# Kernel tuning notes

Measured on AMD Instinct MI355X. Metric: run time of the kernel, lower is better.

Reference implementation:

```python
import jax, jax.numpy as jnp
import numpy as np

N = 100000   # nodes
E = 1600000  # edges
F = 128      # input/hidden dim
C = 3        # classes
G = 64       # graphs in batch


def setup_inputs() -> dict:
    key = jax.random.key(0)
    ks = jax.random.split(key, 12)
    s = 1.0 / np.sqrt(F)
    return {
        "x": jax.random.normal(ks[0], (N, F), dtype=jnp.float32),
        "edge_index": jax.random.randint(ks[1], (2, E), 0, N, dtype=jnp.int64),
        "batch": jnp.sort(jax.random.randint(ks[2], (N,), 0, G, dtype=jnp.int64)),
        "W1": jax.random.normal(ks[3], (F, F), dtype=jnp.float32) * s,
        "b1": jnp.zeros((F,), dtype=jnp.float32),
        "W2": jax.random.normal(ks[4], (F, F), dtype=jnp.float32) * s,
        "b2": jnp.zeros((F,), dtype=jnp.float32),
        "W3": jax.random.normal(ks[5], (F, F), dtype=jnp.float32) * s,
        "b3": jnp.zeros((F,), dtype=jnp.float32),
        "Wc": jax.random.normal(ks[6], (F, C), dtype=jnp.float32) * s,
        "bc": jnp.zeros((C,), dtype=jnp.float32),
    }


def reference(x, edge_index, batch, W1, b1, W2, b2, W3, b3, Wc, bc):
    n = x.shape[0]
    src, dst = edge_index[0], edge_index[1]
    # GCN adds self-loops: A_hat = A + I
    loops = jnp.arange(n, dtype=src.dtype)
    src_a = jnp.concatenate([src, loops])
    dst_a = jnp.concatenate([dst, loops])
    # symmetric normalization D^-1/2 (A+I) D^-1/2 (in-degree incl. self-loop)
    deg = jax.ops.segment_sum(jnp.ones_like(dst_a, dtype=x.dtype), dst_a, num_segments=n)
    dis = jnp.where(deg > 0, jax.lax.rsqrt(deg), 0.0)
    norm = dis[src_a] * dis[dst_a]  # [E+N]

    def gcn_conv(h, W, b):
        h = h @ W                                    # [N, F']
        msg = h[src_a] * norm[:, None]               # gather + scale
        agg = jax.ops.segment_sum(msg, dst_a, num_segments=n)  # scatter-add
        return agg + b

    h = jax.nn.relu(gcn_conv(x, W1, b1))   # dropout = identity in eval mode
    h = jax.nn.relu(gcn_conv(h, W2, b2))
    h = jax.nn.relu(gcn_conv(h, W3, b3))

    # global_mean_pool over graph ids
    sums = jax.ops.segment_sum(h, batch, num_segments=G)
    cnt = jax.ops.segment_sum(jnp.ones((n,), dtype=h.dtype), batch, num_segments=G)
    pooled = sums / jnp.maximum(cnt, 1.0)[:, None]
    return pooled @ Wc + bc
```

## Files before the change

kernel.cpp:

```cpp
#include <hip/hip_runtime.h>
#include <cstdint>
#include <cstddef>

#define FDIM 128
#define CHUNK 4096
#define BSHIFT 8
#define BMASK 255
#define MAXB 512

typedef unsigned short ushort_t;
typedef __attribute__((ext_vector_type(8))) short short8;
typedef __attribute__((ext_vector_type(4))) float floatx4;

__device__ inline ushort_t f2bf(float f) {
  unsigned u = __float_as_uint(f);
  u += 0x7fffu + ((u >> 16) & 1u);
  return (ushort_t)(u >> 16);
}
__device__ inline float bf2f(ushort_t h) {
  return __uint_as_float((unsigned)h << 16);
}

__global__ __launch_bounds__(256) void k_histw(const int* __restrict__ dst, int e,
                                               int nb, int* __restrict__ chunkHist,
                                               int nch,
                                               const float* __restrict__ W1,
                                               const float* __restrict__ W2,
                                               const float* __restrict__ W3,
                                               ushort_t* __restrict__ wsw,
                                               int* __restrict__ counter) {
  if (blockIdx.x >= (unsigned)nch) {
    int b = blockIdx.x - nch;
    if (b == 0 && threadIdx.x == 0) *counter = 0;
    const float* W = (b == 0) ? W1 : (b == 1) ? W2 : W3;
    ushort_t* o = wsw + (size_t)b * 16384;
    for (int idx = threadIdx.x; idx < 16384; idx += 256) {
      int j = idx & 7;
      int lane = (idx >> 3) & 63;
      int ct = (idx >> 9) & 7;
      int kc = idx >> 12;
      int k = kc * 32 + (lane >> 4) * 8 + j;
      int col = (lane & 15) * 8 + ct;
      o[idx] = f2bf(W[k * FDIM + col]);
    }
    return;
  }
  __shared__ int h[MAXB];
  int c = blockIdx.x;
  int base = c * CHUNK;
  int end = min(base + CHUNK, e);
  for (int i = threadIdx.x; i < nb; i += 256) h[i] = 0;
  __syncthreads();
  for (int i = base + threadIdx.x; i < end; i += 256)
    atomicAdd(&h[dst[i] >> BSHIFT], 1);
  __syncthreads();
  for (int b = threadIdx.x; b < nb; b += 256)
    chunkHist[(size_t)c * nb + b] = h[b];
}

__global__ __launch_bounds__(512) void k_scan1(const int* __restrict__ chunkHist,
                                               int nchunks, int nb,
                                               int* __restrict__ chunkOff,
                                               int* __restrict__ bucketTotal,
                                               int* __restrict__ bucketBase,
                                               int* __restrict__ counter) {
  __shared__ int sb[512];
  int b = blockIdx.x;
  int t = threadIdx.x;
  int base = 0;
  for (int c0 = 0; c0 < nchunks; c0 += 512) {
    int c = c0 + t;
    int v = (c < nchunks) ? chunkHist[(size_t)c * nb + b] : 0;
    int x = v;
    sb[t] = x;
    __syncthreads();
    for (int off = 1; off < 512; off <<= 1) {
      int y = (t >= off) ? sb[t - off] : 0;
      __syncthreads();
      x += y;
      sb[t] = x;
      __syncthreads();
    }
    if (c < nchunks) chunkOff[(size_t)c * nb + b] = base + x - v;
    int tileTot = sb[511];
    __syncthreads();
    base += tileTot;
  }
  if (t == 0) {
    bucketTotal[b] = base;
    bucketBase[b] = atomicAdd(counter, base);
  }
}

__global__ __launch_bounds__(256) void k_bin(const int* __restrict__ src,
                                             const int* __restrict__ dst, int e, int nb,
                                             const int* __restrict__ chunkHist,
                                             const int* __restrict__ chunkOff,
                                             const int* __restrict__ bucketBase,
                                             unsigned* __restrict__ binned) {
  __shared__ unsigned sortedL[CHUNK];
  __shared__ int gtarget[CHUNK];
  __shared__ int lbase[MAXB], lcur[MAXB], gbase[MAXB];
  __shared__ int stmp[256];
  int c = blockIdx.x;
  int base = c * CHUNK;
  int end = min(base + CHUNK, e);
  for (int i = threadIdx.x; i < nb; i += 256) {
    lbase[i] = chunkHist[(size_t)c * nb + i];
    gbase[i] = bucketBase[i] + chunkOff[(size_t)c * nb + i];
  }
  __syncthreads();
  int carry = 0;
  for (int i0 = 0; i0 < nb; i0 += 256) {
    int i = i0 + threadIdx.x;
    int v = (i < nb) ? lbase[i] : 0;
    int x = v;
    stmp[threadIdx.x] = x;
    __syncthreads();
    for (int off = 1; off < 256; off <<= 1) {
      int y = (threadIdx.x >= off) ? stmp[threadIdx.x - off] : 0;
      __syncthreads();
      x += y;
      stmp[threadIdx.x] = x;
      __syncthreads();
    }
    if (i < nb) lbase[i] = carry + x - v;
    int tileTot = stmp[255];
    __syncthreads();
    carry += tileTot;
  }
  for (int i = threadIdx.x; i < nb; i += 256) lcur[i] = lbase[i];
  __syncthreads();
  for (int i = base + threadIdx.x; i < end; i += 256) {
    int d = dst[i];
    int sv = src[i];
    int b = d >> BSHIFT;
    int slot = atomicAdd(&lcur[b], 1);
    sortedL[slot] = ((unsigned)sv << BSHIFT) | (unsigned)(d & BMASK);
    gtarget[slot] = gbase[b] + (slot - lbase[b]);
  }
  __syncthreads();
  for (int i = threadIdx.x; i < end - base; i += 256)
    binned[gtarget[i]] = sortedL[i];
}

__global__ __launch_bounds__(256) void k_fill2(const unsigned* __restrict__ binned,
                                               const int* __restrict__ bucketBase,
                                               const int* __restrict__ bucketTotal,
                                               int n,
                                               int* __restrict__ rowStart,
                                               int* __restrict__ deg,
                                               float* __restrict__ dis,
                                               unsigned* __restrict__ colPacked) {
  __shared__ int h[256], sb[256], cur[256];
  int b = blockIdx.x;
  int s0 = bucketBase[b], s1 = s0 + bucketTotal[b];
  int nodeBase = b << BSHIFT;
  int t = threadIdx.x;
  h[t] = 0;
  __syncthreads();
  for (int i = s0 + t; i < s1; i += 256) atomicAdd(&h[binned[i] & BMASK], 1);
  __syncthreads();
  int v = h[t];
  int x = v;
  sb[t] = x;
  __syncthreads();
  for (int off = 1; off < 256; off <<= 1) {
    int y = (t >= off) ? sb[t - off] : 0;
    __syncthreads();
    x += y;
    sb[t] = x;
    __syncthreads();
  }
  int start = s0 + x - v;
  cur[t] = start;
  int node = nodeBase + t;
  if (node < n) {
    rowStart[node] = start;
    deg[node] = v;
    dis[node] = rsqrtf((float)(v + 1));
  }
  __syncthreads();
  for (int i = s0 + t; i < s1; i += 256) {
    unsigned en = binned[i];
    int slot = atomicAdd(&cur[en & BMASK], 1);
    colPacked[slot] = en >> BSHIFT;
  }
}

template <int INBF, int EDGW>
__global__ __launch_bounds__(256) void k_mm(const void* __restrict__ Ain,
                                            const ushort_t* __restrict__ Wsw,
                                            ushort_t* __restrict__ O, int n, int mmb,
                                            unsigned* __restrict__ colPacked, int e,
                                            const float* __restrict__ dis) {
  if (EDGW && blockIdx.x >= (unsigned)mmb) {
    int base = (blockIdx.x - mmb) * 2048 + threadIdx.x;
    for (int k = 0; k < 8; ++k) {
      int i = base + k * 256;
      if (i < e) {
        unsigned p = colPacked[i];
        colPacked[i] = p | ((unsigned)f2bf(dis[p]) << 17);
      }
    }
    return;
  }
  __shared__ ushort_t Bs[16384];
  int tid = threadIdx.x;
  for (int q = tid; q < 2048; q += 256)
    ((uint4*)Bs)[q] = ((const uint4*)Wsw)[q];
  __syncthreads();

  int w = tid >> 6;
  int lane = tid & 63;
  int quad = lane >> 4;
  int l15 = lane & 15;
  int rb = blockIdx.x * 128 + w * 32;
  const float* Af = (const float*)Ain;
  const ushort_t* Ab = (const ushort_t*)Ain;

  int row0 = rb + l15;
  int row1 = rb + 16 + l15;
  bool v0 = row0 < n, v1 = row1 < n;

  floatx4 acc[2][8];
#pragma unroll
  for (int rt = 0; rt < 2; ++rt)
#pragma unroll
    for (int ct = 0; ct < 8; ++ct) acc[rt][ct] = floatx4{0.f, 0.f, 0.f, 0.f};

#pragma unroll
  for (int kc = 0; kc < 4; ++kc) {
    int k0 = kc * 32 + quad * 8;
    short8 a0 = short8{0, 0, 0, 0, 0, 0, 0, 0};
    short8 a1 = short8{0, 0, 0, 0, 0, 0, 0, 0};
    if (INBF) {
      if (v0) a0 = *(const short8*)&Ab[(size_t)row0 * FDIM + k0];
      if (v1) a1 = *(const short8*)&Ab[(size_t)row1 * FDIM + k0];
    } else {
      if (v0) {
        float4 f0 = *(const float4*)&Af[(size_t)row0 * FDIM + k0];
        float4 f1 = *(const float4*)&Af[(size_t)row0 * FDIM + k0 + 4];
        a0 = short8{(short)f2bf(f0.x), (short)f2bf(f0.y), (short)f2bf(f0.z),
                    (short)f2bf(f0.w), (short)f2bf(f1.x), (short)f2bf(f1.y),
                    (short)f2bf(f1.z), (short)f2bf(f1.w)};
      }
      if (v1) {
        float4 f0 = *(const float4*)&Af[(size_t)row1 * FDIM + k0];
        float4 f1 = *(const float4*)&Af[(size_t)row1 * FDIM + k0 + 4];
        a1 = short8{(short)f2bf(f0.x), (short)f2bf(f0.y), (short)f2bf(f0.z),
                    (short)f2bf(f0.w), (short)f2bf(f1.x), (short)f2bf(f1.y),
                    (short)f2bf(f1.z), (short)f2bf(f1.w)};
      }
    }
#pragma unroll
    for (int ct = 0; ct < 8; ++ct) {
      short8 bf = *(const short8*)&Bs[((kc * 8 + ct) * 64 + lane) * 8];
      acc[0][ct] = __builtin_amdgcn_mfma_f32_16x16x32_bf16(a0, bf, acc[0][ct], 0, 0, 0);
      acc[1][ct] = __builtin_amdgcn_mfma_f32_16x16x32_bf16(a1, bf, acc[1][ct], 0, 0, 0);
    }
  }

#pragma unroll
  for (int rt = 0; rt < 2; ++rt) {
#pragma unroll
    for (int i = 0; i < 4; ++i) {
      int row = rb + rt * 16 + quad * 4 + i;
      if (row < n) {
        uint4 pk;
        pk.x = (unsigned)f2bf(acc[rt][0][i]) | ((unsigned)f2bf(acc[rt][1][i]) << 16);
        pk.y = (unsigned)f2bf(acc[rt][2][i]) | ((unsigned)f2bf(acc[rt][3][i]) << 16);
        pk.z = (unsigned)f2bf(acc[rt][4][i]) | ((unsigned)f2bf(acc[rt][5][i]) << 16);
        pk.w = (unsigned)f2bf(acc[rt][6][i]) | ((unsigned)f2bf(acc[rt][7][i]) << 16);
        *(uint4*)&O[(size_t)row * FDIM + l15 * 8] = pk;
      }
    }
  }
}

__global__ __launch_bounds__(256) void k_agg(const ushort_t* __restrict__ Hin,
                                             ushort_t* __restrict__ Hout,
                                             const int* __restrict__ rowStart,
                                             const int* __restrict__ degE,
                                             const unsigned* __restrict__ colPacked,
                                             const float* __restrict__ dis,
                                             const float* __restrict__ bias, int n) {
  int node = blockIdx.x * 8 + (threadIdx.x >> 5);
  int lane = threadIdx.x & 31;
  if (node >= n) return;
  const uint2* hin = (const uint2*)Hin;
  float di = dis[node];
  uint2 su = hin[(size_t)node * 32 + lane];
  float ws = di * di;
  float a0 = ws * __uint_as_float(su.x << 16);
  float a1 = ws * __uint_as_float(su.x & 0xffff0000u);
  float a2 = ws * __uint_as_float(su.y << 16);
  float a3 = ws * __uint_as_float(su.y & 0xffff0000u);
  int s0 = rowStart[node], cnt = degE[node];
  const unsigned* __restrict__ cp = colPacked + s0;

  int j = 0;
  int main8 = cnt & ~7;
  if (main8) {
    unsigned pv[8];
#pragma unroll
    for (int k = 0; k < 8; ++k) pv[k] = cp[k];
    for (;;) {
      uint2 u[8];
#pragma unroll
      for (int k = 0; k < 8; ++k)
        u[k] = hin[(size_t)(pv[k] & 0x1ffffu) * 32 + lane];
      int jn = j + 8;
      bool more = jn < main8;
      unsigned pn[8];
      if (more) {
#pragma unroll
        for (int k = 0; k < 8; ++k) pn[k] = cp[jn + k];
      }
#pragma unroll
      for (int k = 0; k < 8; ++k) {
        float w = di * __uint_as_float((pv[k] >> 17) << 16);
        a0 += w * __uint_as_float(u[k].x << 16);
        a1 += w * __uint_as_float(u[k].x & 0xffff0000u);
        a2 += w * __uint_as_float(u[k].y << 16);
        a3 += w * __uint_as_float(u[k].y & 0xffff0000u);
      }
      j = jn;
      if (!more) break;
#pragma unroll
      for (int k = 0; k < 8; ++k) pv[k] = pn[k];
    }
  }
  if (j + 4 <= cnt) {
    unsigned pv[4];
#pragma unroll
    for (int k = 0; k < 4; ++k) pv[k] = cp[j + k];
    uint2 u[4];
#pragma unroll
    for (int k = 0; k < 4; ++k)
      u[k] = hin[(size_t)(pv[k] & 0x1ffffu) * 32 + lane];
#pragma unroll
    for (int k = 0; k < 4; ++k) {
      float w = di * __uint_as_float((pv[k] >> 17) << 16);
      a0 += w * __uint_as_float(u[k].x << 16);
      a1 += w * __uint_as_float(u[k].x & 0xffff0000u);
      a2 += w * __uint_as_float(u[k].y << 16);
      a3 += w * __uint_as_float(u[k].y & 0xffff0000u);
    }
    j += 4;
  }
  for (; j < cnt; ++j) {
    unsigned pv = cp[j];
    int sidx = (int)(pv & 0x1ffffu);
    float w = di * __uint_as_float((pv >> 17) << 16);
    uint2 u = hin[(size_t)sidx * 32 + lane];
    a0 += w * __uint_as_float(u.x << 16);
    a1 += w * __uint_as_float(u.x & 0xffff0000u);
    a2 += w * __uint_as_float(u.y << 16);
    a3 += w * __uint_as_float(u.y & 0xffff0000u);
  }
  float4 b = ((const float4*)bias)[lane];
  a0 = fmaxf(a0 + b.x, 0.f);
  a1 = fmaxf(a1 + b.y, 0.f);
  a2 = fmaxf(a2 + b.z, 0.f);
  a3 = fmaxf(a3 + b.w, 0.f);
  uint2 o;
  o.x = (unsigned)f2bf(a0) | ((unsigned)f2bf(a1) << 16);
  o.y = (unsigned)f2bf(a2) | ((unsigned)f2bf(a3) << 16);
  ((uint2*)Hout)[(size_t)node * 32 + lane] = o;
}


__device__ inline int lower_bound_batch(const int* __restrict__ batch, int n, int g) {
  int lo = 0, hi = n;
  while (lo < hi) {
    int mid = (lo + hi) >> 1;
    if (batch[mid] < g) lo = mid + 1;
    else hi = mid;
  }
  return lo;
}

__global__ __launch_bounds__(128) void k_pool(const ushort_t* __restrict__ H,
                                              const int* __restrict__ batch, int n,
                                              float* __restrict__ partials,
                                              int g_count) {
  __shared__ int se[2];
  int g = blockIdx.x >> 4;
  int c = blockIdx.x & 15;
  if (threadIdx.x < 2)
    se[threadIdx.x] = lower_bound_batch(batch, n, g + (int)threadIdx.x);
  __syncthreads();
  int s = se[0], e = se[1];
  int chunk = (e - s + 15) >> 4;
  int ns = s + c * chunk;
  int ne = min(ns + chunk, e);
  float acc = 0.f;
  for (int i = ns; i < ne; ++i) acc += bf2f(H[(size_t)i * FDIM + threadIdx.x]);
  partials[((size_t)g * 16 + c) * FDIM + threadIdx.x] = acc;
}

__global__ __launch_bounds__(128) void k_final(const float* __restrict__ partials,
                                               const int* __restrict__ batch, int n,
                                               const float* __restrict__ Wc,
                                               const float* __restrict__ bc,
                                               float* __restrict__ out, int g_count) {
  __shared__ int se[2];
  __shared__ float red[6];
  int t = threadIdx.x;
  int g = blockIdx.x;
  if (t < 2) se[t] = lower_bound_batch(batch, n, g + t);
  __syncthreads();
  float inv = 1.0f / (float)max(se[1] - se[0], 1);
  float s = 0.f;
#pragma unroll
  for (int p = 0; p < 16; ++p) s += partials[((size_t)g * 16 + p) * FDIM + t];
  s *= inv;
#pragma unroll
  for (int c = 0; c < 3; ++c) {
    float v = s * Wc[t * 3 + c];
#pragma unroll
    for (int off = 1; off < 64; off <<= 1) v += __shfl_xor(v, off);
    if ((t & 63) == 0) red[(t >> 6) * 3 + c] = v;
  }
  __syncthreads();
  if (t < 3) out[g * 3 + t] = red[t] + red[3 + t] + bc[t];
}


extern "C" void kernel_launch(void* const* d_in, const int* in_sizes, int n_in,
                              void* d_out, int out_size, void* d_ws, size_t ws_size,
                              hipStream_t stream) {
  const float* x = (const float*)d_in[0];
  const int* edge = (const int*)d_in[1];
  const int* batch = (const int*)d_in[2];
  const float* W1 = (const float*)d_in[3];
  const float* b1 = (const float*)d_in[4];
  const float* W2 = (const float*)d_in[5];
  const float* b2 = (const float*)d_in[6];
  const float* W3 = (const float*)d_in[7];
  const float* b3 = (const float*)d_in[8];
  const float* Wc = (const float*)d_in[9];
  const float* bc = (const float*)d_in[10];
  float* out = (float*)d_out;

  const int N = in_sizes[0] / FDIM;
  const int E = in_sizes[1] / 2;
  const int G = out_size / 3;
  const int* src = edge;
  const int* dst = edge + E;

  const int NCH = (E + CHUNK - 1) / CHUNK;
  const int NB = (N + (1 << BSHIFT) - 1) >> BSHIFT;

  char* ws = (char*)d_ws;
  size_t off = 0;
  auto carve = [&](size_t bytes) -> void* {
    void* p = ws + off;
    off = (off + bytes + 255) & ~(size_t)255;
    return p;
  };
  ushort_t* h0 = (ushort_t*)carve((size_t)N * FDIM * 2);
  ushort_t* h1 = (ushort_t*)carve((size_t)N * FDIM * 2);
  unsigned* colPacked = (unsigned*)carve((size_t)E * 4);
  unsigned* binned = (unsigned*)carve((size_t)E * 4);
  int* chunkHist = (int*)carve((size_t)NCH * NB * 4);
  int* chunkOff = (int*)carve((size_t)NCH * NB * 4);
  int* bucketTotal = (int*)carve((size_t)NB * 4);
  int* bucketBase = (int*)carve((size_t)NB * 4);
  int* counter = (int*)carve(256);
  int* rowStart = (int*)carve((size_t)N * 4);
  int* deg = (int*)carve((size_t)N * 4);
  float* dis = (float*)carve((size_t)N * 4);
  float* partials = (float*)carve((size_t)G * 16 * FDIM * 4);
  ushort_t* wsw = (ushort_t*)carve((size_t)3 * 16384 * 2);
  (void)n_in;
  (void)ws_size;

  k_histw<<<NCH + 3, 256, 0, stream>>>(dst, E, NB, chunkHist, NCH, W1, W2, W3, wsw,
                                       counter);
  k_scan1<<<NB, 512, 0, stream>>>(chunkHist, NCH, NB, chunkOff, bucketTotal,
                                  bucketBase, counter);
  k_bin<<<NCH, 256, 0, stream>>>(src, dst, E, NB, chunkHist, chunkOff, bucketBase,
                                 binned);
  k_fill2<<<NB, 256, 0, stream>>>(binned, bucketBase, bucketTotal, N, rowStart, deg,
                                  dis, colPacked);

  int mmb = (N + 127) / 128;
  int ewb = (E + 2047) / 2048;
  int aggb = (N + 7) / 8;
  k_mm<0, 1><<<mmb + ewb, 256, 0, stream>>>(x, wsw, h0, N, mmb, colPacked, E, dis);
  k_agg<<<aggb, 256, 0, stream>>>(h0, h1, rowStart, deg, colPacked, dis, b1, N);
  k_mm<1, 0><<<mmb, 256, 0, stream>>>(h1, wsw + 16384, h0, N, mmb, nullptr, 0,
                                      nullptr);
  k_agg<<<aggb, 256, 0, stream>>>(h0, h1, rowStart, deg, colPacked, dis, b2, N);
  k_mm<1, 0><<<mmb, 256, 0, stream>>>(h1, wsw + 32768, h0, N, mmb, nullptr, 0,
                                      nullptr);
  k_agg<<<aggb, 256, 0, stream>>>(h0, h1, rowStart, deg, colPacked, dis, b3, N);

  k_pool<<<G * 16, 128, 0, stream>>>(h1, batch, N, partials, G);
  k_final<<<G, 128, 0, stream>>>(partials, batch, N, Wc, bc, out, G);
}
```

Baseline: 417.3 us.

## Fuse GCN aggregation with next layer's matmul via LDS-staged tile

Adds k_fagg, which aggregates neighbor features for 128 nodes per block into a swizzled LDS tile, then multiplies that tile by the next layer's weights with MFMA. It replaces the separate agg and mm kernels for layers 1 and 2. This removes a global write and read of the intermediate node features plus two launches per layer. In exchange each block needs 64KB of LDS and 512 threads, which limits occupancy during the latency-bound gather phase.

After: 435.6 us. 1.04x slower.

```diff
diff --git a/kernel.cpp b/kernel.cpp
--- a/kernel.cpp
+++ b/kernel.cpp
@@ -274,6 +274,144 @@
         pk.w = (unsigned)f2bf(acc[rt][6][i]) | ((unsigned)f2bf(acc[rt][7][i]) << 16);
         *(uint4*)&O[(size_t)row * FDIM + l15 * 8] = pk;
       }
+    }
+  }
+}
+
+__global__ __launch_bounds__(512, 4) void k_fagg(
+    const ushort_t* __restrict__ Hin, const ushort_t* __restrict__ Wsw,
+    ushort_t* __restrict__ O, const int* __restrict__ rowStart,
+    const int* __restrict__ degE, const unsigned* __restrict__ colPacked,
+    const float* __restrict__ dis, const float* __restrict__ bias, int n) {
+  __shared__ ushort_t As[16384];
+  __shared__ ushort_t Bs[16384];
+  int tid = threadIdx.x;
+  for (int q = tid; q < 2048; q += 512)
+    ((uint4*)Bs)[q] = ((const uint4*)Wsw)[q];
+
+  int w = tid >> 6;
+  int lane = tid & 63;
+  int hw = lane >> 5;
+  int lane32 = lane & 31;
+  int rb = blockIdx.x * 128;
+  const uint2* hin = (const uint2*)Hin;
+  float4 bvec = ((const float4*)bias)[lane32];
+
+  for (int p = 0; p < 8; ++p) {
+    int lrow = w * 16 + p * 2 + hw;
+    int node = rb + lrow;
+    float a0 = 0.f, a1 = 0.f, a2 = 0.f, a3 = 0.f;
+    if (node < n) {
+      float di = dis[node];
+      uint2 su = hin[(size_t)node * 32 + lane32];
+      float ws = di * di;
+      a0 = ws * __uint_as_float(su.x << 16);
+      a1 = ws * __uint_as_float(su.x & 0xffff0000u);
+      a2 = ws * __uint_as_float(su.y << 16);
+      a3 = ws * __uint_as_float(su.y & 0xffff0000u);
+      int s0 = rowStart[node], cnt = degE[node];
+      const unsigned* __restrict__ cp = colPacked + s0;
+      int j = 0;
+      int main8 = cnt & ~7;
+      if (main8) {
+        unsigned pv[8];
+#pragma unroll
+        for (int k = 0; k < 8; ++k) pv[k] = cp[k];
+        for (;;) {
+          uint2 u[8];
+#pragma unroll
+          for (int k = 0; k < 8; ++k)
+            u[k] = hin[(size_t)(pv[k] & 0x1ffffu) * 32 + lane32];
+          int jn = j + 8;
+          bool more = jn < main8;
+          unsigned pn[8];
+          if (more) {
+#pragma unroll
+            for (int k = 0; k < 8; ++k) pn[k] = cp[jn + k];
+          }
+#pragma unroll
+          for (int k = 0; k < 8; ++k) {
+            float wv = di * __uint_as_float((pv[k] >> 17) << 16);
+            a0 += wv * __uint_as_float(u[k].x << 16);
+            a1 += wv * __uint_as_float(u[k].x & 0xffff0000u);
+            a2 += wv * __uint_as_float(u[k].y << 16);
+            a3 += wv * __uint_as_float(u[k].y & 0xffff0000u);
+          }
+          j = jn;
+          if (!more) break;
+#pragma unroll
+          for (int k = 0; k < 8; ++k) pv[k] = pn[k];
+        }
+      }
+      if (j + 4 <= cnt) {
+        unsigned pv[4];
+#pragma unroll
+        for (int k = 0; k < 4; ++k) pv[k] = cp[j + k];
+        uint2 u[4];
+#pragma unroll
+        for (int k = 0; k < 4; ++k)
+          u[k] = hin[(size_t)(pv[k] & 0x1ffffu) * 32 + lane32];
+#pragma unroll
+        for (int k = 0; k < 4; ++k) {
+          float wv = di * __uint_as_float((pv[k] >> 17) << 16);
+          a0 += wv * __uint_as_float(u[k].x << 16);
+          a1 += wv * __uint_as_float(u[k].x & 0xffff0000u);
+          a2 += wv * __uint_as_float(u[k].y << 16);
+          a3 += wv * __uint_as_float(u[k].y & 0xffff0000u);
+        }
+        j += 4;
+      }
+      for (; j < cnt; ++j) {
+        unsigned pv = cp[j];
+        int sidx = (int)(pv & 0x1ffffu);
+        float wv = di * __uint_as_float((pv >> 17) << 16);
+        uint2 u = hin[(size_t)sidx * 32 + lane32];
+        a0 += wv * __uint_as_float(u.x << 16);
+        a1 += wv * __uint_as_float(u.x & 0xffff0000u);
+        a2 += wv * __uint_as_float(u.y << 16);
+        a3 += wv * __uint_as_float(u.y & 0xffff0000u);
+      }
+      a0 = fmaxf(a0 + bvec.x, 0.f);
+      a1 = fmaxf(a1 + bvec.y, 0.f);
+      a2 = fmaxf(a2 + bvec.z, 0.f);
+      a3 = fmaxf(a3 + bvec.w, 0.f);
+    }
+    uint2 o;
+    o.x = (unsigned)f2bf(a0) | ((unsigned)f2bf(a1) << 16);
+    o.y = (unsigned)f2bf(a2) | ((unsigned)f2bf(a3) << 16);
+    int byte = lrow * 256 + lane32 * 8;
+    byte ^= (lrow & 7) << 4;
+    *(uint2*)((char*)As + byte) = o;
+  }
+  __syncthreads();
+
+  int quad = lane >> 4;
+  int l15 = lane & 15;
+  floatx4 acc[8];
+#pragma unroll
+  for (int ct = 0; ct < 8; ++ct) acc[ct] = floatx4{0.f, 0.f, 0.f, 0.f};
+  int lrow = w * 16 + l15;
+#pragma unroll
+  for (int kc = 0; kc < 4; ++kc) {
+    int byte = lrow * 256 + kc * 64 + quad * 16;
+    byte ^= (lrow & 7) << 4;
+    short8 a = *(const short8*)((const char*)As + byte);
+#pragma unroll
+    for (int ct = 0; ct < 8; ++ct) {
+      short8 bf = *(const short8*)&Bs[((kc * 8 + ct) * 64 + lane) * 8];
+      acc[ct] = __builtin_amdgcn_mfma_f32_16x16x32_bf16(a, bf, acc[ct], 0, 0, 0);
+    }
+  }
+#pragma unroll
+  for (int i = 0; i < 4; ++i) {
+    int row = rb + w * 16 + quad * 4 + i;
+    if (row < n) {
+      uint4 pk;
+      pk.x = (unsigned)f2bf(acc[0][i]) | ((unsigned)f2bf(acc[1][i]) << 16);
+      pk.y = (unsigned)f2bf(acc[2][i]) | ((unsigned)f2bf(acc[3][i]) << 16);
+      pk.z = (unsigned)f2bf(acc[4][i]) | ((unsigned)f2bf(acc[5][i]) << 16);
+      pk.w = (unsigned)f2bf(acc[6][i]) | ((unsigned)f2bf(acc[7][i]) << 16);
+      *(uint4*)&O[(size_t)row * FDIM + l15 * 8] = pk;
     }
   }
 }
@@ -489,13 +627,12 @@
   int mmb = (N + 127) / 128;
   int ewb = (E + 2047) / 2048;
   int aggb = (N + 7) / 8;
+  int fb = (N + 127) / 128;
   k_mm<0, 1><<<mmb + ewb, 256, 0, stream>>>(x, wsw, h0, N, mmb, colPacked, E, dis);
-  k_agg<<<aggb, 256, 0, stream>>>(h0, h1, rowStart, deg, colPacked, dis, b1, N);
-  k_mm<1, 0><<<mmb, 256, 0, stream>>>(h1, wsw + 16384, h0, N, mmb, nullptr, 0,
-                                      nullptr);
-  k_agg<<<aggb, 256, 0, stream>>>(h0, h1, rowStart, deg, colPacked, dis, b2, N);
-  k_mm<1, 0><<<mmb, 256, 0, stream>>>(h1, wsw + 32768, h0, N, mmb, nullptr, 0,
-                                      nullptr);
+  k_fagg<<<fb, 512, 0, stream>>>(h0, wsw + 16384, h1, rowStart, deg, colPacked, dis,
+                                 b1, N);
+  k_fagg<<<fb, 512, 0, stream>>>(h1, wsw + 32768, h0, rowStart, deg, colPacked, dis,
+                                 b2, N);
   k_agg<<<aggb, 256, 0, stream>>>(h0, h1, rowStart, deg, colPacked, dis, b3, N);
 
   k_pool<<<G * 16, 128, 0, stream>>>(h1, batch, N, partials, G);
```

## Replace two-level bucket sort CSR build with global atomic counting sort

Applied to the files above, without the earlier changes.

Builds the destination-sorted CSR with global atomics instead of the chunked two-pass bucket sort. It counts in-degree with one atomic per edge, does a two-level block scan over nodes to get row starts, and scatters source ids through per-node atomic cursors. This drops the chunk histogram, per-bucket scan and binned intermediate buffer, at the cost of heavily contended global atomics and random scattered writes. Edge order within a row is now nondeterministic, so summation order can vary between runs.

Measured after the change: 581.7 us. 1.39x slower.

```diff
diff --git a/kernel.cpp b/kernel.cpp
--- a/kernel.cpp
+++ b/kernel.cpp
@@ -3,10 +3,6 @@
 #include <cstddef>
 
 #define FDIM 128
-#define CHUNK 4096
-#define BSHIFT 8
-#define BMASK 255
-#define MAXB 512
 
 typedef unsigned short ushort_t;
 typedef __attribute__((ext_vector_type(8))) short short8;
@@ -21,17 +17,15 @@
   return __uint_as_float((unsigned)h << 16);
 }
 
-__global__ __launch_bounds__(256) void k_histw(const int* __restrict__ dst, int e,
-                                               int nb, int* __restrict__ chunkHist,
-                                               int nch,
+
+__global__ __launch_bounds__(256) void k_zerow(int n, int zb,
+                                               int* __restrict__ deg,
                                                const float* __restrict__ W1,
                                                const float* __restrict__ W2,
                                                const float* __restrict__ W3,
-                                               ushort_t* __restrict__ wsw,
-                                               int* __restrict__ counter) {
-  if (blockIdx.x >= (unsigned)nch) {
-    int b = blockIdx.x - nch;
-    if (b == 0 && threadIdx.x == 0) *counter = 0;
+                                               ushort_t* __restrict__ wsw) {
+  if (blockIdx.x >= (unsigned)zb) {
+    int b = blockIdx.x - zb;
     const float* W = (b == 0) ? W1 : (b == 1) ? W2 : W3;
     ushort_t* o = wsw + (size_t)b * 16384;
     for (int idx = threadIdx.x; idx < 16384; idx += 256) {
@@ -45,124 +39,43 @@
     }
     return;
   }
-  __shared__ int h[MAXB];
-  int c = blockIdx.x;
-  int base = c * CHUNK;
-  int end = min(base + CHUNK, e);
-  for (int i = threadIdx.x; i < nb; i += 256) h[i] = 0;
-  __syncthreads();
-  for (int i = base + threadIdx.x; i < end; i += 256)
-    atomicAdd(&h[dst[i] >> BSHIFT], 1);
-  __syncthreads();
-  for (int b = threadIdx.x; b < nb; b += 256)
-    chunkHist[(size_t)c * nb + b] = h[b];
-}
-
-__global__ __launch_bounds__(512) void k_scan1(const int* __restrict__ chunkHist,
-                                               int nchunks, int nb,
-                                               int* __restrict__ chunkOff,
-                                               int* __restrict__ bucketTotal,
-                                               int* __restrict__ bucketBase,
-                                               int* __restrict__ counter) {
-  __shared__ int sb[512];
-  int b = blockIdx.x;
+  int i0 = blockIdx.x * 1024 + threadIdx.x * 4;
+  if (i0 + 3 < n) {
+    *(int4*)&deg[i0] = int4{0, 0, 0, 0};
+  } else {
+    for (int k = 0; k < 4; ++k)
+      if (i0 + k < n) deg[i0 + k] = 0;
+  }
+}
+
+__global__ __launch_bounds__(256) void k_deg(const int* __restrict__ dst, int e,
+                                             int* __restrict__ deg) {
+  int base = blockIdx.x * 2048 + threadIdx.x;
+#pragma unroll
+  for (int k = 0; k < 8; ++k) {
+    int i = base + k * 256;
+    if (i < e) atomicAdd(&deg[dst[i]], 1);
+  }
+}
+
+__global__ __launch_bounds__(256) void k_scan_blk(const int* __restrict__ deg, int n,
+                                                  int* __restrict__ rowLocal,
+                                                  int* __restrict__ blockSum,
+                                                  float* __restrict__ dis) {
+  __shared__ int sb[256];
   int t = threadIdx.x;
-  int base = 0;
-  for (int c0 = 0; c0 < nchunks; c0 += 512) {
-    int c = c0 + t;
-    int v = (c < nchunks) ? chunkHist[(size_t)c * nb + b] : 0;
-    int x = v;
-    sb[t] = x;
-    __syncthreads();
-    for (int off = 1; off < 512; off <<= 1) {
-      int y = (t >= off) ? sb[t - off] : 0;
-      __syncthreads();
-      x += y;
-      sb[t] = x;
-      __syncthreads();
-    }
-    if (c < nchunks) chunkOff[(size_t)c * nb + b] = base + x - v;
-    int tileTot = sb[511];
-    __syncthreads();
-    base += tileTot;
-  }
-  if (t == 0) {
-    bucketTotal[b] = base;
-    bucketBase[b] = atomicAdd(counter, base);
-  }
-}
-
-__global__ __launch_bounds__(256) void k_bin(const int* __restrict__ src,
-                                             const int* __restrict__ dst, int e, int nb,
-                                             const int* __restrict__ chunkHist,
-                                             const int* __restrict__ chunkOff,
-                                             const int* __restrict__ bucketBase,
-                                             unsigned* __restrict__ binned) {
-  __shared__ unsigned sortedL[CHUNK];
-  __shared__ int gtarget[CHUNK];
-  __shared__ int lbase[MAXB], lcur[MAXB], gbase[MAXB];
-  __shared__ int stmp[256];
-  int c = blockIdx.x;
-  int base = c * CHUNK;
-  int end = min(base + CHUNK, e);
-  for (int i = threadIdx.x; i < nb; i += 256) {
-    lbase[i] = chunkHist[(size_t)c * nb + i];
-    gbase[i] = bucketBase[i] + chunkOff[(size_t)c * nb + i];
-  }
-  __syncthreads();
-  int carry = 0;
-  for (int i0 = 0; i0 < nb; i0 += 256) {
-    int i = i0 + threadIdx.x;
-    int v = (i < nb) ? lbase[i] : 0;
-    int x = v;
-    stmp[threadIdx.x] = x;
-    __syncthreads();
-    for (int off = 1; off < 256; off <<= 1) {
-      int y = (threadIdx.x >= off) ? stmp[threadIdx.x - off] : 0;
-      __syncthreads();
-      x += y;
-      stmp[threadIdx.x] = x;
-      __syncthreads();
-    }
-    if (i < nb) lbase[i] = carry + x - v;
-    int tileTot = stmp[255];
-    __syncthreads();
-    carry += tileTot;
-  }
-  for (int i = threadIdx.x; i < nb; i += 256) lcur[i] = lbase[i];
-  __syncthreads();
-  for (int i = base + threadIdx.x; i < end; i += 256) {
-    int d = dst[i];
-    int sv = src[i];
-    int b = d >> BSHIFT;
-    int slot = atomicAdd(&lcur[b], 1);
-    sortedL[slot] = ((unsigned)sv << BSHIFT) | (unsigned)(d & BMASK);
-    gtarget[slot] = gbase[b] + (slot - lbase[b]);
-  }
-  __syncthreads();
-  for (int i = threadIdx.x; i < end - base; i += 256)
-    binned[gtarget[i]] = sortedL[i];
-}
-
-__global__ __launch_bounds__(256) void k_fill2(const unsigned* __restrict__ binned,
-                                               const int* __restrict__ bucketBase,
-                                               const int* __restrict__ bucketTotal,
-                                               int n,
-                                               int* __restrict__ rowStart,
-                                               int* __restrict__ deg,
-                                               float* __restrict__ dis,
-                                               unsigned* __restrict__ colPacked) {
-  __shared__ int h[256], sb[256], cur[256];
-  int b = blockIdx.x;
-  int s0 = bucketBase[b], s1 = s0 + bucketTotal[b];
-  int nodeBase = b << BSHIFT;
-  int t = threadIdx.x;
-  h[t] = 0;
-  __syncthreads();
-  for (int i = s0 + t; i < s1; i += 256) atomicAdd(&h[binned[i] & BMASK], 1);
-  __syncthreads();
-  int v = h[t];
-  int x = v;
+  int i0 = blockIdx.x * 1024 + t * 4;
+  int4 d = int4{0, 0, 0, 0};
+  if (i0 + 3 < n) {
+    d = *(const int4*)&deg[i0];
+  } else {
+    if (i0 + 0 < n) d.x = deg[i0 + 0];
+    if (i0 + 1 < n) d.y = deg[i0 + 1];
+    if (i0 + 2 < n) d.z = deg[i0 + 2];
+    if (i0 + 3 < n) d.w = deg[i0 + 3];
+  }
+  int s4 = d.x + d.y + d.z + d.w;
+  int x = s4;
   sb[t] = x;
   __syncthreads();
   for (int off = 1; off < 256; off <<= 1) {
@@ -172,19 +85,87 @@
     sb[t] = x;
     __syncthreads();
   }
-  int start = s0 + x - v;
-  cur[t] = start;
-  int node = nodeBase + t;
-  if (node < n) {
-    rowStart[node] = start;
-    deg[node] = v;
-    dis[node] = rsqrtf((float)(v + 1));
-  }
-  __syncthreads();
-  for (int i = s0 + t; i < s1; i += 256) {
-    unsigned en = binned[i];
-    int slot = atomicAdd(&cur[en & BMASK], 1);
-    colPacked[slot] = en >> BSHIFT;
+  int base = x - s4;
+  int4 rl;
+  rl.x = base;
+  rl.y = base + d.x;
+  rl.z = base + d.x + d.y;
+  rl.w = base + d.x + d.y + d.z;
+  if (i0 + 3 < n) {
+    *(int4*)&rowLocal[i0] = rl;
+    float4 dv;
+    dv.x = rsqrtf((float)(d.x + 1));
+    dv.y = rsqrtf((float)(d.y + 1));
+    dv.z = rsqrtf((float)(d.z + 1));
+    dv.w = rsqrtf((float)(d.w + 1));
+    *(float4*)&dis[i0] = dv;
+  } else {
+    int dd[4] = {d.x, d.y, d.z, d.w};
+    int rr[4] = {rl.x, rl.y, rl.z, rl.w};
+    for (int k = 0; k < 4; ++k)
+      if (i0 + k < n) {
+        rowLocal[i0 + k] = rr[k];
+        dis[i0 + k] = rsqrtf((float)(dd[k] + 1));
+      }
+  }
+  if (t == 255) blockSum[blockIdx.x] = x;
+}
+
+__global__ __launch_bounds__(256) void k_finrow(const int* __restrict__ rowLocal,
+                                                const int* __restrict__ blockSum,
+                                                int nsb, int n,
+                                                int* __restrict__ rowStart,
+                                                int* __restrict__ cur) {
+  __shared__ int sb[256];
+  __shared__ int soff;
+  int t = threadIdx.x;
+  int v = (t < nsb) ? blockSum[t] : 0;
+  int x = v;
+  sb[t] = x;
+  __syncthreads();
+  for (int off = 1; off < 256; off <<= 1) {
+    int y = (t >= off) ? sb[t - off] : 0;
+    __syncthreads();
+    x += y;
+    sb[t] = x;
+    __syncthreads();
+  }
+  if (t == (int)blockIdx.x) soff = x - v;
+  __syncthreads();
+  int off0 = soff;
+  int i0 = blockIdx.x * 1024 + t * 4;
+  if (i0 + 3 < n) {
+    int4 rl = *(const int4*)&rowLocal[i0];
+    rl.x += off0;
+    rl.y += off0;
+    rl.z += off0;
+    rl.w += off0;
+    *(int4*)&rowStart[i0] = rl;
+    *(int4*)&cur[i0] = rl;
+  } else {
+    for (int k = 0; k < 4; ++k)
+      if (i0 + k < n) {
+        int r = rowLocal[i0 + k] + off0;
+        rowStart[i0 + k] = r;
+        cur[i0 + k] = r;
+      }
+  }
+}
+
+__global__ __launch_bounds__(256) void k_scatter(const int* __restrict__ src,
+                                                 const int* __restrict__ dst, int e,
+                                                 int* __restrict__ cur,
+                                                 unsigned* __restrict__ colPacked) {
+  int base = blockIdx.x * 2048 + threadIdx.x;
+#pragma unroll
+  for (int k = 0; k < 8; ++k) {
+    int i = base + k * 256;
+    if (i < e) {
+      int d = dst[i];
+      int s = src[i];
+      int slot = atomicAdd(&cur[d], 1);
+      colPacked[slot] = (unsigned)s;
+    }
   }
 }
 
@@ -450,8 +431,9 @@
   const int* src = edge;
   const int* dst = edge + E;
 
-  const int NCH = (E + CHUNK - 1) / CHUNK;
-  const int NB = (N + (1 << BSHIFT) - 1) >> BSHIFT;
+  const int ZB = (N + 1023) / 1024;
+  const int NSB = (N + 1023) / 1024;
+  const int EB = (E + 2047) / 2048;
 
   char* ws = (char*)d_ws;
   size_t off = 0;
@@ -463,28 +445,22 @@
   ushort_t* h0 = (ushort_t*)carve((size_t)N * FDIM * 2);
   ushort_t* h1 = (ushort_t*)carve((size_t)N * FDIM * 2);
   unsigned* colPacked = (unsigned*)carve((size_t)E * 4);
-  unsigned* binned = (unsigned*)carve((size_t)E * 4);
-  int* chunkHist = (int*)carve((size_t)NCH * NB * 4);
-  int* chunkOff = (int*)carve((size_t)NCH * NB * 4);
-  int* bucketTotal = (int*)carve((size_t)NB * 4);
-  int* bucketBase = (int*)carve((size_t)NB * 4);
-  int* counter = (int*)carve(256);
   int* rowStart = (int*)carve((size_t)N * 4);
+  int* rowLocal = (int*)carve((size_t)N * 4);
+  int* cur = (int*)carve((size_t)N * 4);
   int* deg = (int*)carve((size_t)N * 4);
   float* dis = (float*)carve((size_t)N * 4);
+  int* blockSum = (int*)carve(256 * 4);
   float* partials = (float*)carve((size_t)G * 16 * FDIM * 4);
   ushort_t* wsw = (ushort_t*)carve((size_t)3 * 16384 * 2);
   (void)n_in;
   (void)ws_size;
 
-  k_histw<<<NCH + 3, 256, 0, stream>>>(dst, E, NB, chunkHist, NCH, W1, W2, W3, wsw,
-                                       counter);
-  k_scan1<<<NB, 512, 0, stream>>>(chunkHist, NCH, NB, chunkOff, bucketTotal,
-                                  bucketBase, counter);
-  k_bin<<<NCH, 256, 0, stream>>>(src, dst, E, NB, chunkHist, chunkOff, bucketBase,
-                                 binned);
-  k_fill2<<<NB, 256, 0, stream>>>(binned, bucketBase, bucketTotal, N, rowStart, deg,
-                                  dis, colPacked);
+  k_zerow<<<ZB + 3, 256, 0, stream>>>(N, ZB, deg, W1, W2, W3, wsw);
+  k_deg<<<EB, 256, 0, stream>>>(dst, E, deg);
+  k_scan_blk<<<NSB, 256, 0, stream>>>(deg, N, rowLocal, blockSum, dis);
+  k_finrow<<<NSB, 256, 0, stream>>>(rowLocal, blockSum, NSB, N, rowStart, cur);
+  k_scatter<<<EB, 256, 0, stream>>>(src, dst, E, cur, colPacked);
 
   int mmb = (N + 127) / 128;
   int ewb = (E + 2047) / 2048;
```

## Fuse global mean pooling into final aggregation kernel via atomics

Applied to the files above, without the earlier changes.

The third aggregation kernel now accumulates its ReLU outputs directly into per-graph sums, first through shared-memory atomics when a block's 8 nodes share one graph and otherwise through global atomics. This removes the separate pooling kernel and the write and re-read of the final bf16 hidden tensor. The partials buffer shrinks to one row per graph and is zeroed in an extra block of the first kernel. The cost is contention on 64 graph rows from about 12.5k blocks doing global float atomics, and the summation order becomes nondeterministic.

Measured after the change: 412.2 us. No clear change (-1.2%).

```diff
diff --git a/kernel.cpp b/kernel.cpp
--- a/kernel.cpp
+++ b/kernel.cpp
@@ -28,9 +28,15 @@
                                                const float* __restrict__ W2,
                                                const float* __restrict__ W3,
                                                ushort_t* __restrict__ wsw,
-                                               int* __restrict__ counter) {
+                                               int* __restrict__ counter,
+                                               float* __restrict__ partials,
+                                               int g_count) {
   if (blockIdx.x >= (unsigned)nch) {
     int b = blockIdx.x - nch;
+    if (b == 3) {
+      for (int i = threadIdx.x; i < g_count * FDIM; i += 256) partials[i] = 0.f;
+      return;
+    }
     if (b == 0 && threadIdx.x == 0) *counter = 0;
     const float* W = (b == 0) ? W1 : (b == 1) ? W2 : W3;
     ushort_t* o = wsw + (size_t)b * 16384;
@@ -278,96 +284,134 @@
   }
 }
 
+template <int POOL>
 __global__ __launch_bounds__(256) void k_agg(const ushort_t* __restrict__ Hin,
                                              ushort_t* __restrict__ Hout,
                                              const int* __restrict__ rowStart,
                                              const int* __restrict__ degE,
                                              const unsigned* __restrict__ colPacked,
                                              const float* __restrict__ dis,
-                                             const float* __restrict__ bias, int n) {
-  int node = blockIdx.x * 8 + (threadIdx.x >> 5);
-  int lane = threadIdx.x & 31;
-  if (node >= n) return;
-  const uint2* hin = (const uint2*)Hin;
-  float di = dis[node];
-  uint2 su = hin[(size_t)node * 32 + lane];
-  float ws = di * di;
-  float a0 = ws * __uint_as_float(su.x << 16);
-  float a1 = ws * __uint_as_float(su.x & 0xffff0000u);
-  float a2 = ws * __uint_as_float(su.y << 16);
-  float a3 = ws * __uint_as_float(su.y & 0xffff0000u);
-  int s0 = rowStart[node], cnt = degE[node];
-  const unsigned* __restrict__ cp = colPacked + s0;
-
-  int j = 0;
-  int main8 = cnt & ~7;
-  if (main8) {
-    unsigned pv[8];
-#pragma unroll
-    for (int k = 0; k < 8; ++k) pv[k] = cp[k];
-    for (;;) {
-      uint2 u[8];
-#pragma unroll
-      for (int k = 0; k < 8; ++k)
+                                             const float* __restrict__ bias, int n,
+                                             const int* __restrict__ batch,
+                                             float* __restrict__ partials) {
+  int tid = threadIdx.x;
+  int node = blockIdx.x * 8 + (tid >> 5);
+  int lane = tid & 31;
+  bool act = node < n;
+  if (!POOL && !act) return;
+  float a0 = 0.f, a1 = 0.f, a2 = 0.f, a3 = 0.f;
+  if (act) {
+    const uint2* hin = (const uint2*)Hin;
+    float di = dis[node];
+    uint2 su = hin[(size_t)node * 32 + lane];
+    float ws = di * di;
+    a0 = ws * __uint_as_float(su.x << 16);
+    a1 = ws * __uint_as_float(su.x & 0xffff0000u);
+    a2 = ws * __uint_as_float(su.y << 16);
+    a3 = ws * __uint_as_float(su.y & 0xffff0000u);
+    int s0 = rowStart[node], cnt = degE[node];
+    const unsigned* __restrict__ cp = colPacked + s0;
+
+    int j = 0;
+    int main8 = cnt & ~7;
+    if (main8) {
+      unsigned pv[8];
+#pragma unroll
+      for (int k = 0; k < 8; ++k) pv[k] = cp[k];
+      for (;;) {
+        uint2 u[8];
+#pragma unroll
+        for (int k = 0; k < 8; ++k)
+          u[k] = hin[(size_t)(pv[k] & 0x1ffffu) * 32 + lane];
+        int jn = j + 8;
+        bool more = jn < main8;
+        unsigned pn[8];
+        if (more) {
+#pragma unroll
+          for (int k = 0; k < 8; ++k) pn[k] = cp[jn + k];
+        }
+#pragma unroll
+        for (int k = 0; k < 8; ++k) {
+          float w = di * __uint_as_float((pv[k] >> 17) << 16);
+          a0 += w * __uint_as_float(u[k].x << 16);
+          a1 += w * __uint_as_float(u[k].x & 0xffff0000u);
+          a2 += w * __uint_as_float(u[k].y << 16);
+          a3 += w * __uint_as_float(u[k].y & 0xffff0000u);
+        }
+        j = jn;
+        if (!more) break;
+#pragma unroll
+        for (int k = 0; k < 8; ++k) pv[k] = pn[k];
+      }
+    }
+    if (j + 4 <= cnt) {
+      unsigned pv[4];
+#pragma unroll
+      for (int k = 0; k < 4; ++k) pv[k] = cp[j + k];
+      uint2 u[4];
+#pragma unroll
+      for (int k = 0; k < 4; ++k)
         u[k] = hin[(size_t)(pv[k] & 0x1ffffu) * 32 + lane];
-      int jn = j + 8;
-      bool more = jn < main8;
-      unsigned pn[8];
-      if (more) {
-#pragma unroll
-        for (int k = 0; k < 8; ++k) pn[k] = cp[jn + k];
-      }
-#pragma unroll
-      for (int k = 0; k < 8; ++k) {
+#pragma unroll
+      for (int k = 0; k < 4; ++k) {
         float w = di * __uint_as_float((pv[k] >> 17) << 16);
         a0 += w * __uint_as_float(u[k].x << 16);
         a1 += w * __uint_as_float(u[k].x & 0xffff0000u);
         a2 += w * __uint_as_float(u[k].y << 16);
         a3 += w * __uint_as_float(u[k].y & 0xffff0000u);
       }
-      j = jn;
-      if (!more) break;
-#pragma unroll
-      for (int k = 0; k < 8; ++k) pv[k] = pn[k];
-    }
-  }
-  if (j + 4 <= cnt) {
-    unsigned pv[4];
-#pragma unroll
-    for (int k = 0; k < 4; ++k) pv[k] = cp[j + k];
-    uint2 u[4];
-#pragma unroll
-    for (int k = 0; k < 4; ++k)
-      u[k] = hin[(size_t)(pv[k] & 0x1ffffu) * 32 + lane];
-#pragma unroll
-    for (int k = 0; k < 4; ++k) {
-      float w = di * __uint_as_float((pv[k] >> 17) << 16);
-      a0 += w * __uint_as_float(u[k].x << 16);
-      a1 += w * __uint_as_float(u[k].x & 0xffff0000u);
-      a2 += w * __uint_as_float(u[k].y << 16);
-      a3 += w * __uint_as_float(u[k].y & 0xffff0000u);
-    }
-    j += 4;
-  }
-  for (; j < cnt; ++j) {
-    unsigned pv = cp[j];
-    int sidx = (int)(pv & 0x1ffffu);
-    float w = di * __uint_as_float((pv >> 17) << 16);
-    uint2 u = hin[(size_t)sidx * 32 + lane];
-    a0 += w * __uint_as_float(u.x << 16);
-    a1 += w * __uint_as_float(u.x & 0xffff0000u);
-    a2 += w * __uint_as_float(u.y << 16);
-    a3 += w * __uint_as_float(u.y & 0xffff0000u);
-  }
-  float4 b = ((const float4*)bias)[lane];
-  a0 = fmaxf(a0 + b.x, 0.f);
-  a1 = fmaxf(a1 + b.y, 0.f);
-  a2 = fmaxf(a2 + b.z, 0.f);
-  a3 = fmaxf(a3 + b.w, 0.f);
-  uint2 o;
-  o.x = (unsigned)f2bf(a0) | ((unsigned)f2bf(a1) << 16);
-  o.y = (unsigned)f2bf(a2) | ((unsigned)f2bf(a3) << 16);
-  ((uint2*)Hout)[(size_t)node * 32 + lane] = o;
+      j += 4;
+    }
+    for (; j < cnt; ++j) {
+      unsigned pv = cp[j];
+      int sidx = (int)(pv & 0x1ffffu);
+      float w = di * __uint_as_float((pv >> 17) << 16);
+      uint2 u = hin[(size_t)sidx * 32 + lane];
+      a0 += w * __uint_as_float(u.x << 16);
+      a1 += w * __uint_as_float(u.x & 0xffff0000u);
+      a2 += w * __uint_as_float(u.y << 16);
+      a3 += w * __uint_as_float(u.y & 0xffff0000u);
+    }
+    float4 b = ((const float4*)bias)[lane];
+    a0 = fmaxf(a0 + b.x, 0.f);
+    a1 = fmaxf(a1 + b.y, 0.f);
+    a2 = fmaxf(a2 + b.z, 0.f);
+    a3 = fmaxf(a3 + b.w, 0.f);
+    if (!POOL) {
+      uint2 o;
+      o.x = (unsigned)f2bf(a0) | ((unsigned)f2bf(a1) << 16);
+      o.y = (unsigned)f2bf(a2) | ((unsigned)f2bf(a3) << 16);
+      ((uint2*)Hout)[(size_t)node * 32 + lane] = o;
+    }
+  }
+  if (POOL) {
+    __shared__ float pool_s[FDIM];
+    __shared__ int sg;
+    int base = blockIdx.x * 8;
+    if (tid == 0) {
+      int lastn = min(base + 7, n - 1);
+      int g0 = batch[base];
+      sg = (g0 == batch[lastn]) ? g0 : -1;
+    }
+    if (tid < FDIM) pool_s[tid] = 0.f;
+    __syncthreads();
+    if (sg >= 0) {
+      if (act) {
+        atomicAdd(&pool_s[lane * 4 + 0], a0);
+        atomicAdd(&pool_s[lane * 4 + 1], a1);
+        atomicAdd(&pool_s[lane * 4 + 2], a2);
+        atomicAdd(&pool_s[lane * 4 + 3], a3);
+      }
+      __syncthreads();
+      if (tid < FDIM) atomicAdd(&partials[(size_t)sg * FDIM + tid], pool_s[tid]);
+    } else if (act) {
+      int gn = batch[node];
+      atomicAdd(&partials[(size_t)gn * FDIM + lane * 4 + 0], a0);
+      atomicAdd(&partials[(size_t)gn * FDIM + lane * 4 + 1], a1);
+      atomicAdd(&partials[(size_t)gn * FDIM + lane * 4 + 2], a2);
+      atomicAdd(&partials[(size_t)gn * FDIM + lane * 4 + 3], a3);
+    }
+  }
 }
 
 
@@ -379,25 +423,6 @@
     else hi = mid;
   }
   return lo;
-}
-
-__global__ __launch_bounds__(128) void k_pool(const ushort_t* __restrict__ H,
-                                              const int* __restrict__ batch, int n,
-                                              float* __restrict__ partials,
-                                              int g_count) {
-  __shared__ int se[2];
-  int g = blockIdx.x >> 4;
-  int c = blockIdx.x & 15;
-  if (threadIdx.x < 2)
-    se[threadIdx.x] = lower_bound_batch(batch, n, g + (int)threadIdx.x);
-  __syncthreads();
-  int s = se[0], e = se[1];
-  int chunk = (e - s + 15) >> 4;
-  int ns = s + c * chunk;
-  int ne = min(ns + chunk, e);
-  float acc = 0.f;
-  for (int i = ns; i < ne; ++i) acc += bf2f(H[(size_t)i * FDIM + threadIdx.x]);
-  partials[((size_t)g * 16 + c) * FDIM + threadIdx.x] = acc;
 }
 
 __global__ __launch_bounds__(128) void k_final(const float* __restrict__ partials,
@@ -412,10 +437,7 @@
   if (t < 2) se[t] = lower_bound_batch(batch, n, g + t);
   __syncthreads();
   float inv = 1.0f / (float)max(se[1] - se[0], 1);
-  float s = 0.f;
-#pragma unroll
-  for (int p = 0; p < 16; ++p) s += partials[((size_t)g * 16 + p) * FDIM + t];
-  s *= inv;
+  float s = partials[(size_t)g * FDIM + t] * inv;
 #pragma unroll
   for (int c = 0; c < 3; ++c) {
     float v = s * Wc[t * 3 + c];
@@ -472,13 +494,13 @@
   int* rowStart = (int*)carve((size_t)N * 4);
   int* deg = (int*)carve((size_t)N * 4);
   float* dis = (float*)carve((size_t)N * 4);
-  float* partials = (float*)carve((size_t)G * 16 * FDIM * 4);
+  float* partials = (float*)carve((size_t)G * FDIM * 4);
   ushort_t* wsw = (ushort_t*)carve((size_t)3 * 16384 * 2);
   (void)n_in;
   (void)ws_size;
 
-  k_histw<<<NCH + 3, 256, 0, stream>>>(dst, E, NB, chunkHist, NCH, W1, W2, W3, wsw,
-                                       counter);
+  k_histw<<<NCH + 4, 256, 0, stream>>>(dst, E, NB, chunkHist, NCH, W1, W2, W3, wsw,
+                                       counter, partials, G);
   k_scan1<<<NB, 512, 0, stream>>>(chunkHist, NCH, NB, chunkOff, bucketTotal,
                                   bucketBase, counter);
   k_bin<<<NCH, 256, 0, stream>>>(src, dst, E, NB, chunkHist, chunkOff, bucketBase,
@@ -490,14 +512,16 @@
   int ewb = (E + 2047) / 2048;
   int aggb = (N + 7) / 8;
   k_mm<0, 1><<<mmb + ewb, 256, 0, stream>>>(x, wsw, h0, N, mmb, colPacked, E, dis);
-  k_agg<<<aggb, 256, 0, stream>>>(h0, h1, rowStart, deg, colPacked, dis, b1, N);
+  k_agg<0><<<aggb, 256, 0, stream>>>(h0, h1, rowStart, deg, colPacked, dis, b1, N,
+                                     nullptr, nullptr);
   k_mm<1, 0><<<mmb, 256, 0, stream>>>(h1, wsw + 16384, h0, N, mmb, nullptr, 0,
                                       nullptr);
-  k_agg<<<aggb, 256, 0, stream>>>(h0, h1, rowStart, deg, colPacked, dis, b2, N);
+  k_agg<0><<<aggb, 256, 0, stream>>>(h0, h1, rowStart, deg, colPacked, dis, b2, N,
+                                     nullptr, nullptr);
   k_mm<1, 0><<<mmb, 256, 0, stream>>>(h1, wsw + 32768, h0, N, mmb, nullptr, 0,
                                       nullptr);
-  k_agg<<<aggb, 256, 0, stream>>>(h0, h1, rowStart, deg, colPacked, dis, b3, N);
-
-  k_pool<<<G * 16, 128, 0, stream>>>(h1, batch, N, partials, G);
+  k_agg<1><<<aggb, 256, 0, stream>>>(h0, h1, rowStart, deg, colPacked, dis, b3, N,
+                                     batch, partials);
+
   k_final<<<G, 128, 0, stream>>>(partials, batch, N, Wc, bc, out, G);
 }
```
